# Optimization experiments

Hardware: AMD Instinct MI355X
Metric: run time of the kernel (lower is better)

## Reference

```python
import jax, jax.numpy as jnp
import numpy as np

OUT_H, OUT_W = 512, 512
BATCH, CHANNELS = 64, 3


def setup_inputs() -> dict:
    key = jax.random.key(0)
    k1, k2 = jax.random.split(key)
    U = jax.random.normal(k1, (BATCH, OUT_H, OUT_W, CHANNELS), dtype=jnp.float32)
    theta = jax.random.normal(k2, (BATCH, 1), dtype=jnp.float32)
    return {"U": U, "theta": theta}


def reference(U, theta):
    B = U.shape[0]
    H, W = OUT_H, OUT_W
    # normalized sampling grid [H*W, 3] with homogeneous coordinate
    gx, gy = jnp.meshgrid(jnp.linspace(-1.0, 1.0, W), jnp.linspace(-1.0, 1.0, H))
    grid = jnp.stack([gx, gy, jnp.ones_like(gx)], axis=-1).reshape(H * W, 3)
    # rotation-only affine matrix [B, 2, 3]
    cos_t, sin_t, z = jnp.cos(theta), jnp.sin(theta), jnp.zeros_like(theta)
    rot = jnp.concatenate([cos_t, -sin_t, z, sin_t, cos_t, z], axis=1).reshape(B, 2, 3)
    # transformed source coords [B, H*W, 2]
    T_g = jnp.einsum('bij,nj->bni', rot, grid)
    x = (T_g[..., 0] + 1.0) * (W - 1) / 2.0
    y = (T_g[..., 1] + 1.0) * (H - 1) / 2.0
    x0f = jnp.floor(x).astype(jnp.int32)
    y0f = jnp.floor(y).astype(jnp.int32)
    x0 = jnp.clip(x0f, 0, W - 1)
    x1 = jnp.clip(x0f + 1, 0, W - 1)
    y0 = jnp.clip(y0f, 0, H - 1)
    y1 = jnp.clip(y0f + 1, 0, H - 1)
    # 4-corner gathers, batched: [B, H*W, C]
    gather = jax.vmap(lambda u, yy, xx: u[yy, xx])
    Ia = gather(U, y0, x0)
    Ib = gather(U, y1, x0)
    Ic = gather(U, y0, x1)
    Id = gather(U, y1, x1)
    x0_f, x1_f = x0.astype(jnp.float32), x1.astype(jnp.float32)
    y0_f, y1_f = y0.astype(jnp.float32), y1.astype(jnp.float32)
    wa = (x1_f - x) * (y1_f - y)
    wb = (x1_f - x) * (y - y0_f)
    wc = (x - x0_f) * (y1_f - y)
    wd = (x - x0_f) * (y - y0_f)
    out = (wa[..., None] * Ia + wb[..., None] * Ib
           + wc[..., None] * Ic + wd[..., None] * Id)
    return out.reshape(B, H, W, -1)
```

## Files before the change

kernel.cpp:

```cpp
#include <hip/hip_runtime.h>

#define OUT_H 512
#define OUT_W 512
#define BATCH 64
#define CHANS 3

#define WROWS 46
#define WPX   46
#define RDW   138
#define PITCH 139
#define LSZ   (WROWS * PITCH)
#define IDXMAX 6249

__global__ __launch_bounds__(256) void st_bilinear_kernel(
    const float* __restrict__ U,
    const float* __restrict__ theta,
    float* __restrict__ out)
{
    __shared__ float smf[LSZ];

    int blk  = blockIdx.x;
    int lblk = (blk & 7) * 2048 + (blk >> 3);

    int b  = lblk >> 8;
    int t  = lblk & 255;
    int i0 = (t >> 4) << 5;
    int j0 = (t & 15) << 5;

    int tid = threadIdx.x;

    float tt = theta[__builtin_amdgcn_readfirstlane(b)];
    float s, c;
    __sincosf(tt, &s, &c);

    const float scale = 2.0f / 511.0f;
    float gx0 = (float)j0 * scale - 1.0f;
    float gy0 = (float)i0 * scale - 1.0f;
    float xb0 = (c * gx0 - s * gy0 + 1.0f) * 255.5f;
    float yb0 = (s * gx0 + c * gy0 + 1.0f) * 255.5f;

    float xmin = xb0 + fminf(0.0f, 31.0f * c) + fminf(0.0f, -31.0f * s);
    float ymin = yb0 + fminf(0.0f, 31.0f * s) + fminf(0.0f,  31.0f * c);

    int bx0 = min(max((int)floorf(xmin), 0), OUT_W - 1);
    int by0 = min(max((int)floorf(ymin), 0), OUT_H - 1);
    int bx_load = min(bx0, OUT_W - WPX);
    int by_load = min(by0, OUT_H - WROWS);

    const float* Ub = U + (size_t)b * (OUT_H * OUT_W * CHANS);
    const float* gb = Ub + ((size_t)by_load * OUT_W + bx_load) * CHANS;

    float4 va[7];
#pragma unroll
    for (int it = 0; it < 7; ++it) {
        int u = tid + 256 * it;
        if (it < 6 || u < 46 * 35) {
            int r  = u / 35;
            int cc = u - r * 35;
            int dw = min(4 * cc, 134);
            va[it] = *(const float4*)(gb + (size_t)r * (OUT_W * CHANS) + dw);
        }
    }
#pragma unroll
    for (int it = 0; it < 7; ++it) {
        int u = tid + 256 * it;
        if (it < 6 || u < 46 * 35) {
            int r  = u / 35;
            int cc = u - r * 35;
            int dw = min(4 * cc, 134);
            int base = r * PITCH + dw;
            float4 v = va[it];
            if (cc < 34) {
                smf[base + 0] = v.x; smf[base + 1] = v.y;
                smf[base + 2] = v.z; smf[base + 3] = v.w;
            } else {
                smf[base + 2] = v.z; smf[base + 3] = v.w;
            }
        }
    }
    __syncthreads();

    int il = tid >> 3;
    int jb = (tid & 7) << 2;
    float xr = xb0 + c * (float)jb - s * (float)il;
    float yr = yb0 + s * (float)jb + c * (float)il;
    int Koff = by_load * PITCH + bx_load * 3;

    float o[12];
#pragma unroll
    for (int p = 0; p < 4; ++p) {
        float x = fmaf(c, (float)p, xr);
        float y = fmaf(s, (float)p, yr);

        int ix = __float2int_rd(x);
        int iy = __float2int_rd(y);
        float fx = x - (float)ix;
        float fy = y - (float)iy;

        int idx = iy * PITCH + ix * 3 - Koff;
        idx = min(max(idx, 0), IDXMAX);

        const float* lp = smf + idx;
        float a0 = lp[0], a1 = lp[1], a2 = lp[2];
        float c0 = lp[3], c1 = lp[4], c2 = lp[5];
        float b0 = lp[PITCH + 0], b1 = lp[PITCH + 1], b2 = lp[PITCH + 2];
        float d0 = lp[PITCH + 3], d1 = lp[PITCH + 4], d2 = lp[PITCH + 5];

        float t0 = fmaf(fx, c0 - a0, a0);
        float t1 = fmaf(fx, c1 - a1, a1);
        float t2 = fmaf(fx, c2 - a2, a2);
        float u0 = fmaf(fx, d0 - b0, b0);
        float u1 = fmaf(fx, d1 - b1, b1);
        float u2 = fmaf(fx, d2 - b2, b2);
        float r0 = fmaf(fy, u0 - t0, t0);
        float r1 = fmaf(fy, u1 - t1, t1);
        float r2 = fmaf(fy, u2 - t2, t2);

        bool valid = (x >= 0.0f) && (x < 511.0f) && (y >= 0.0f) && (y < 511.0f);
        o[p * 3 + 0] = valid ? r0 : 0.0f;
        o[p * 3 + 1] = valid ? r1 : 0.0f;
        o[p * 3 + 2] = valid ? r2 : 0.0f;
    }

    float* po = out + (((size_t)b * OUT_H + (i0 + il)) * OUT_W + (j0 + jb)) * CHANS;
    ((float4*)po)[0] = make_float4(o[0], o[1], o[2],  o[3]);
    ((float4*)po)[1] = make_float4(o[4], o[5], o[6],  o[7]);
    ((float4*)po)[2] = make_float4(o[8], o[9], o[10], o[11]);
}

extern "C" void kernel_launch(void* const* d_in, const int* in_sizes, int n_in,
                              void* d_out, int out_size, void* d_ws, size_t ws_size,
                              hipStream_t stream) {
    const float* U     = (const float*)d_in[0];
    const float* theta = (const float*)d_in[1];
    float* out = (float*)d_out;

    int blocks = BATCH * (OUT_H / 32) * (OUT_W / 32);
    st_bilinear_kernel<<<blocks, 256, 0, stream>>>(U, theta, out);
}
```

Baseline: 108.0 us.

## Stage tile in LDS as packed fp16 pixels and interpolate with half2

Converts the staged source window to fp16, packing each RGB pixel into an 8-byte slot with a skewed 64-slot row pitch, and performs bilinear interpolation using half2 FMAs. This cuts LDS footprint and the number of LDS reads per sample (four 64-bit loads instead of twelve scalar loads) and should reduce bank conflicts. It trades output precision (fp16 rounding of inputs and weights) and replaces float4 global loads with float2 plus scalar loads over a slightly larger 48x48 window.

```diff
diff --git a/kernel.cpp b/kernel.cpp
--- a/kernel.cpp
+++ b/kernel.cpp
@@ -1,23 +1,22 @@
 #include <hip/hip_runtime.h>
+#include <hip/hip_fp16.h>
 
 #define OUT_H 512
 #define OUT_W 512
 #define BATCH 64
 #define CHANS 3
 
-#define WROWS 46
-#define WPX   46
-#define RDW   138
-#define PITCH 139
-#define LSZ   (WROWS * PITCH)
-#define IDXMAX 6249
+#define WROWS 48
+#define WPX   48
+#define SLOTP 64
+#define NSLOT (WROWS * SLOTP)
 
 __global__ __launch_bounds__(256) void st_bilinear_kernel(
     const float* __restrict__ U,
     const float* __restrict__ theta,
     float* __restrict__ out)
 {
-    __shared__ float smf[LSZ];
+    __shared__ uint2 sm[NSLOT];
 
     int blk  = blockIdx.x;
     int lblk = (blk & 7) * 2048 + (blk >> 3);
@@ -50,33 +49,28 @@
     const float* Ub = U + (size_t)b * (OUT_H * OUT_W * CHANS);
     const float* gb = Ub + ((size_t)by_load * OUT_W + bx_load) * CHANS;
 
-    float4 va[7];
+    float2 lc01[9];
+    float  lc2[9];
 #pragma unroll
-    for (int it = 0; it < 7; ++it) {
-        int u = tid + 256 * it;
-        if (it < 6 || u < 46 * 35) {
-            int r  = u / 35;
-            int cc = u - r * 35;
-            int dw = min(4 * cc, 134);
-            va[it] = *(const float4*)(gb + (size_t)r * (OUT_W * CHANS) + dw);
-        }
+    for (int k = 0; k < 9; ++k) {
+        unsigned q = (unsigned)tid + 256u * k;
+        unsigned r  = q / 48u;
+        unsigned lx = q - r * 48u;
+        const float* p = gb + (size_t)r * (OUT_W * CHANS) + lx * 3u;
+        lc01[k] = *(const float2*)p;
+        lc2[k]  = p[2];
     }
 #pragma unroll
-    for (int it = 0; it < 7; ++it) {
-        int u = tid + 256 * it;
-        if (it < 6 || u < 46 * 35) {
-            int r  = u / 35;
-            int cc = u - r * 35;
-            int dw = min(4 * cc, 134);
-            int base = r * PITCH + dw;
-            float4 v = va[it];
-            if (cc < 34) {
-                smf[base + 0] = v.x; smf[base + 1] = v.y;
-                smf[base + 2] = v.z; smf[base + 3] = v.w;
-            } else {
-                smf[base + 2] = v.z; smf[base + 3] = v.w;
-            }
-        }
+    for (int k = 0; k < 9; ++k) {
+        unsigned q = (unsigned)tid + 256u * k;
+        unsigned r  = q / 48u;
+        unsigned lx = q - r * 48u;
+        __half2 h01 = __floats2half2_rn(lc01[k].x, lc01[k].y);
+        __half2 h2  = __floats2half2_rn(lc2[k], 0.0f);
+        uint2 v;
+        v.x = *(const unsigned int*)&h01;
+        v.y = *(const unsigned int*)&h2;
+        sm[r * SLOTP + lx + (r & 15u)] = v;
     }
     __syncthreads();
 
@@ -84,7 +78,6 @@
     int jb = (tid & 7) << 2;
     float xr = xb0 + c * (float)jb - s * (float)il;
     float yr = yb0 + s * (float)jb + c * (float)il;
-    int Koff = by_load * PITCH + bx_load * 3;
 
     float o[12];
 #pragma unroll
@@ -97,29 +90,34 @@
         float fx = x - (float)ix;
         float fy = y - (float)iy;
 
-        int idx = iy * PITCH + ix * 3 - Koff;
-        idx = min(max(idx, 0), IDXMAX);
+        int lx = min(max(ix - bx_load, 0), WPX - 2);
+        int ly = min(max(iy - by_load, 0), WROWS - 2);
 
-        const float* lp = smf + idx;
-        float a0 = lp[0], a1 = lp[1], a2 = lp[2];
-        float c0 = lp[3], c1 = lp[4], c2 = lp[5];
-        float b0 = lp[PITCH + 0], b1 = lp[PITCH + 1], b2 = lp[PITCH + 2];
-        float d0 = lp[PITCH + 3], d1 = lp[PITCH + 4], d2 = lp[PITCH + 5];
+        int p0 = ly * SLOTP + lx + (ly & 15);
+        int p1 = (ly + 1) * SLOTP + lx + ((ly + 1) & 15);
 
-        float t0 = fmaf(fx, c0 - a0, a0);
-        float t1 = fmaf(fx, c1 - a1, a1);
-        float t2 = fmaf(fx, c2 - a2, a2);
-        float u0 = fmaf(fx, d0 - b0, b0);
-        float u1 = fmaf(fx, d1 - b1, b1);
-        float u2 = fmaf(fx, d2 - b2, b2);
-        float r0 = fmaf(fy, u0 - t0, t0);
-        float r1 = fmaf(fy, u1 - t1, t1);
-        float r2 = fmaf(fy, u2 - t2, t2);
+        uint2 A0 = sm[p0], A1 = sm[p0 + 1];
+        uint2 B0 = sm[p1], B1 = sm[p1 + 1];
+
+        __half2 fx2 = __float2half2_rn(fx);
+        __half2 fy2 = __float2half2_rn(fy);
+
+        __half2 a01 = *(const __half2*)&A0.x, a2 = *(const __half2*)&A0.y;
+        __half2 c01 = *(const __half2*)&A1.x, c2 = *(const __half2*)&A1.y;
+        __half2 b01 = *(const __half2*)&B0.x, b2 = *(const __half2*)&B0.y;
+        __half2 d01 = *(const __half2*)&B1.x, d2 = *(const __half2*)&B1.y;
+
+        __half2 t01 = __hfma2(fx2, __hsub2(c01, a01), a01);
+        __half2 t2  = __hfma2(fx2, __hsub2(c2,  a2),  a2);
+        __half2 u01 = __hfma2(fx2, __hsub2(d01, b01), b01);
+        __half2 u2  = __hfma2(fx2, __hsub2(d2,  b2),  b2);
+        __half2 r01 = __hfma2(fy2, __hsub2(u01, t01), t01);
+        __half2 r2  = __hfma2(fy2, __hsub2(u2,  t2),  t2);
 
         bool valid = (x >= 0.0f) && (x < 511.0f) && (y >= 0.0f) && (y < 511.0f);
-        o[p * 3 + 0] = valid ? r0 : 0.0f;
-        o[p * 3 + 1] = valid ? r1 : 0.0f;
-        o[p * 3 + 2] = valid ? r2 : 0.0f;
+        o[p * 3 + 0] = valid ? __low2float(r01)  : 0.0f;
+        o[p * 3 + 1] = valid ? __high2float(r01) : 0.0f;
+        o[p * 3 + 2] = valid ? __low2float(r2)   : 0.0f;
     }
 
     float* po = out + (((size_t)b * OUT_H + (i0 + il)) * OUT_W + (j0 + jb)) * CHANS;
```

Result: faster. 103.8 us (-3.9%).
